# Kernel tuning notes

Measured on AMD Instinct MI355X. Metric: run time of the kernel, lower is better.

## Reference

```python
import jax, jax.numpy as jnp
import numpy as np

N_NODES = 50000


def gcn_conv(x, W, b, row, col, num_nodes):
    """PyG-style GCNConv: out = D^{-1/2}(A+I)D^{-1/2} (x @ W) + b.

    row/col already include self-loops. x: [N, Fin], W: [Fin, Fout].
    """
    h = x @ W  # [N, Fout]
    deg = jax.ops.segment_sum(jnp.ones_like(col, dtype=h.dtype), col,
                              num_segments=num_nodes)  # in-degree incl. self-loop
    dinv = jnp.where(deg > 0, jax.lax.rsqrt(deg), 0.0)
    norm = dinv[row] * dinv[col]  # [E]
    msgs = h[row] * norm[:, None]  # gather + scale, [E, Fout]
    out = jax.ops.segment_sum(msgs, col, num_segments=num_nodes)  # scatter-add
    return out + b


def setup_inputs() -> dict:
    key = jax.random.key(0)
    k1, k2, k3, k4 = jax.random.split(key, 4)
    Fin, Fh, Fout = 128, 128, 64
    E = 800000
    x = jax.random.normal(k1, (N_NODES, Fin), dtype=jnp.float32)
    edge_index = jax.random.randint(k2, (2, E), 0, N_NODES, dtype=jnp.int64)
    # Glorot-ish init for weights
    W1 = jax.random.normal(k3, (Fin, Fh), dtype=jnp.float32) / np.sqrt(Fin)
    b1 = jnp.zeros((Fh,), dtype=jnp.float32)
    W2 = jax.random.normal(k4, (Fh, Fout), dtype=jnp.float32) / np.sqrt(Fh)
    b2 = jnp.zeros((Fout,), dtype=jnp.float32)
    return {"x": x, "edge_index": edge_index, "W1": W1, "b1": b1,
            "W2": W2, "b2": b2}


def reference(x, edge_index, W1, b1, W2, b2):
    n = x.shape[0]
    # add self-loops once (shared by both conv layers)
    loops = jnp.arange(n, dtype=edge_index.dtype)
    row = jnp.concatenate([edge_index[0], loops])
    col = jnp.concatenate([edge_index[1], loops])
    h = jax.nn.relu(gcn_conv(x, W1, b1, row, col, n))
    # dropout(p=0.5) is identity in eval mode (self.training == False)
    return gcn_conv(h, W2, b2, row, col, n)
```

## Files before the change

### kernel.cpp

```cpp
#include <hip/hip_runtime.h>


constexpr int KD = 128;
constexpr int CHUNK = 2048;
constexpr int BCAP = 6144;

using short8  = __attribute__((ext_vector_type(8))) short;
using float4v = __attribute__((ext_vector_type(4))) float;
using uint4v  = __attribute__((ext_vector_type(4))) unsigned int;


__device__ __forceinline__ unsigned short f2bf(float f) {
    unsigned int u = __float_as_uint(f);
    u = (u + 0x7fffu + ((u >> 16) & 1u)) >> 16;
    return (unsigned short)u;
}

__device__ __forceinline__ float2 bfpair(unsigned int u) {
    float2 f;
    f.x = __uint_as_float(u << 16);
    f.y = __uint_as_float(u & 0xffff0000u);
    return f;
}

__device__ __forceinline__ unsigned int packbf(float x, float y) {
    return (unsigned int)f2bf(x) | ((unsigned int)f2bf(y) << 16);
}

__device__ __forceinline__ void bfsplit(float x, unsigned short& h, unsigned short& l) {
    h = f2bf(x);
    float fh = __uint_as_float((unsigned int)h << 16);
    l = f2bf(x - fh);
}

__global__ __launch_bounds__(256) void scatter_setup(
        const int* __restrict__ row, const int* __restrict__ col,
        int* gcur, unsigned int* __restrict__ bpack, int E, int NBS,
        const float* __restrict__ W1, unsigned short* __restrict__ Wth1,
        unsigned short* __restrict__ Wtl1,
        const float* __restrict__ W2, unsigned short* __restrict__ Wth2,
        unsigned short* __restrict__ Wtl2) {
    __shared__ int lh[256];
    __shared__ int lbase[256];

    if ((int)blockIdx.x >= NBS) {
        int id = ((int)blockIdx.x - NBS) * 256 + threadIdx.x;
        unsigned short h, l;
        if (id < 16384) {
            int k = id >> 7, n = id & 127;
            bfsplit(W1[id], h, l);
            Wth1[n * KD + k] = h;
            Wtl1[n * KD + k] = l;
        } else {
            int id2 = id - 16384;
            int k = id2 >> 6, n = id2 & 63;
            bfsplit(W2[id2], h, l);
            Wth2[n * KD + k] = h;
            Wtl2[n * KD + k] = l;
        }
        return;
    }

    lh[threadIdx.x] = 0;
    __syncthreads();
    int base = (int)blockIdx.x * CHUNK;
#pragma unroll
    for (int r = 0; r < CHUNK / 256; ++r) {
        int e = base + r * 256 + threadIdx.x;
        if (e < E) atomicAdd(&lh[col[e] >> 8], 1);
    }
    __syncthreads();
    int c0 = lh[threadIdx.x];
    lbase[threadIdx.x] = c0 ? (threadIdx.x * BCAP + atomicAdd(&gcur[threadIdx.x], c0)) : 0;
    __syncthreads();
    lh[threadIdx.x] = 0;
    __syncthreads();
#pragma unroll
    for (int r = 0; r < CHUNK / 256; ++r) {
        int e = base + r * 256 + threadIdx.x;
        if (e < E) {
            int c = col[e];
            int b = c >> 8;
            int slot = lbase[b] + atomicAdd(&lh[b], 1);
            bpack[slot] = ((unsigned int)row[e] << 16) | (unsigned int)c;
        }
    }
}

__global__ __launch_bounds__(256) void csr_and_gemm1(
        const unsigned int* __restrict__ bpack, const int* __restrict__ gcur,
        int* __restrict__ rowptrS, float* __restrict__ dinv,
        unsigned short* __restrict__ srow, int N, int E, int NBUCKET,
        const float* __restrict__ X,
        const unsigned short* __restrict__ Wth,
        const unsigned short* __restrict__ Wtl,
        unsigned short* __restrict__ G) {
    __shared__ int s[256];
    __shared__ int lh[1024];
    __shared__ int lcur[1024];
    __shared__ int sh_bstart;

    if ((int)blockIdx.x < NBUCKET) {
        int b = blockIdx.x;
        int t = threadIdx.x;
        int cntb = gcur[t];
        s[t] = cntb;
        __syncthreads();
        for (int off = 1; off < 256; off <<= 1) {
            int tv = (t >= off) ? s[t - off] : 0;
            __syncthreads();
            s[t] += tv;
            __syncthreads();
        }
        if (t == b) sh_bstart = s[t] - cntb;
        if (b == 0 && t == 0) rowptrS[4 * N] = E;
#pragma unroll
        for (int k = 0; k < 4; ++k) lh[t * 4 + k] = 0;
        __syncthreads();
        int bstart = sh_bstart;
        int nE = gcur[b];
        int base = b * BCAP;
        for (int i = t; i < nE; i += 256) {
            unsigned int p = bpack[base + i];
            atomicAdd(&lh[(p & 255) * 4 + (p >> 30)], 1);
        }
        __syncthreads();
        int e0 = lh[t * 4], e1 = lh[t * 4 + 1], e2 = lh[t * 4 + 2], e3 = lh[t * 4 + 3];
        int v = e0 + e1 + e2 + e3;
        s[t] = v;
        __syncthreads();
        for (int off = 1; off < 256; off <<= 1) {
            int tv = (t >= off) ? s[t - off] : 0;
            __syncthreads();
            s[t] += tv;
            __syncthreads();
        }
        int myStart = bstart + s[t] - v;
        int node = (b << 8) + t;
        if (node < N) {
            rowptrS[node * 4 + 0] = myStart;
            rowptrS[node * 4 + 1] = myStart + e0;
            rowptrS[node * 4 + 2] = myStart + e0 + e1;
            rowptrS[node * 4 + 3] = myStart + e0 + e1 + e2;
            dinv[node] = rsqrtf(1.0f + (float)v);
        }
        lcur[t * 4 + 0] = myStart;
        lcur[t * 4 + 1] = myStart + e0;
        lcur[t * 4 + 2] = myStart + e0 + e1;
        lcur[t * 4 + 3] = myStart + e0 + e1 + e2;
        __syncthreads();
        for (int i = t; i < nE; i += 256) {
            unsigned int p = bpack[base + i];
            int slot = atomicAdd(&lcur[(p & 255) * 4 + (p >> 30)], 1);
            srow[slot] = (unsigned short)(p >> 16);
        }
    } else {
        constexpr int FOUT = 128, NT = 8;
        int wave = threadIdx.x >> 6;
        int lane = threadIdx.x & 63;
        int row0 = (((int)blockIdx.x - NBUCKET) * 4 + wave) * 16;
        if (row0 >= N) return;
        int m = lane & 15;
        int quad = lane >> 4;

        float4v acc[NT];
#pragma unroll
        for (int ct = 0; ct < NT; ++ct) acc[ct] = (float4v){0.f, 0.f, 0.f, 0.f};

        const float* xrow = X + (size_t)(row0 + m) * KD + quad * 8;

#pragma unroll
        for (int ks = 0; ks < 4; ++ks) {
            float4 xa = *(const float4*)(xrow + ks * 32);
            float4 xb = *(const float4*)(xrow + ks * 32 + 4);
            float xs[8] = {xa.x, xa.y, xa.z, xa.w, xb.x, xb.y, xb.z, xb.w};
            short8 ah, al;
#pragma unroll
            for (int j = 0; j < 8; ++j) {
                unsigned short h, l;
                bfsplit(xs[j], h, l);
                ah[j] = (short)h;
                al[j] = (short)l;
            }
            int koff = ks * 32 + quad * 8;
#pragma unroll
            for (int ct = 0; ct < NT; ++ct) {
                short8 bh = *(const short8*)(Wth + (size_t)(ct * 16 + m) * KD + koff);
                short8 bl = *(const short8*)(Wtl + (size_t)(ct * 16 + m) * KD + koff);
                acc[ct] = __builtin_amdgcn_mfma_f32_16x16x32_bf16(ah, bh, acc[ct], 0, 0, 0);
                acc[ct] = __builtin_amdgcn_mfma_f32_16x16x32_bf16(al, bh, acc[ct], 0, 0, 0);
                acc[ct] = __builtin_amdgcn_mfma_f32_16x16x32_bf16(ah, bl, acc[ct], 0, 0, 0);
            }
        }

#pragma unroll
        for (int r = 0; r < 4; ++r) {
            int row = row0 + quad * 4 + r;
#pragma unroll
            for (int ct = 0; ct < NT; ++ct) {
                G[(size_t)row * FOUT + ct * 16 + m] = f2bf(acc[ct][r]);
            }
        }
    }
}

__global__ __launch_bounds__(256, 4) void gather128_gemm2_seg(
        const int* __restrict__ rowptrS,
        const unsigned short* __restrict__ srow,
        const unsigned int* __restrict__ G,
        const float* __restrict__ dinv,
        const float* __restrict__ bias,
        const unsigned short* __restrict__ Wth,
        const unsigned short* __restrict__ Wtl,
        unsigned short* __restrict__ G2,
        int N, int E) {
    __shared__ unsigned int lhs[16 * 64];
    __shared__ float ldinv[16];

    int lane = threadIdx.x & 63;
    int l16  = threadIdx.x & 15;
    int q    = threadIdx.x >> 4;
    const uint4v* Gv = (const uint4v*)G;

    float acc[4][8];
    float dns[4];

#pragma unroll
    for (int t = 0; t < 4; ++t) {
        int node = (int)blockIdx.x * 64 + t * 16 + q;
        int nc = (node < N) ? node : 0;
        float dn = dinv[nc];
        dns[t] = dn;
        uint4v s0 = Gv[(size_t)nc * 16 + l16];
        float2 v0 = bfpair(s0[0]), v1 = bfpair(s0[1]);
        float2 v2 = bfpair(s0[2]), v3 = bfpair(s0[3]);
        acc[t][0] = v0.x * dn; acc[t][1] = v0.y * dn;
        acc[t][2] = v1.x * dn; acc[t][3] = v1.y * dn;
        acc[t][4] = v2.x * dn; acc[t][5] = v2.y * dn;
        acc[t][6] = v3.x * dn; acc[t][7] = v3.y * dn;
    }

    for (int sgm = 0; sgm < 4; ++sgm) {
#pragma unroll
        for (int t = 0; t < 4; ++t) {
            int node = (int)blockIdx.x * 64 + t * 16 + q;
            bool valid = node < N;
            int nc = valid ? node : 0;
            int beg = rowptrS[nc * 4 + sgm];
            int end = rowptrS[nc * 4 + sgm + 1];
            int deg = valid ? (end - beg) : 0;
            int dm = max(deg, __shfl_xor(deg, 16));
            dm = max(dm, __shfl_xor(dm, 32));
            for (int w = 0; w < dm; w += 16) {
                int li = w + l16;
                li = (li < deg) ? li : (deg > 0 ? deg - 1 : 0);
                li += beg;
                li = (li < E) ? li : (E - 1);
                int rv = (int)srow[li];
                float dv = dinv[rv];
                int lim = dm - w;
                for (int g = 0; g < 16 && g < lim; g += 4) {
                    uint4v u[4];
                    float dr[4];
#pragma unroll
                    for (int j = 0; j < 4; ++j) {
                        int src = (lane & 48) | (g + j);
                        int r = __shfl(rv, src);
                        dr[j] = __shfl(dv, src);
                        u[j] = Gv[(size_t)r * 16 + l16];
                    }
                    float sa[8] = {0.f, 0.f, 0.f, 0.f, 0.f, 0.f, 0.f, 0.f};
#pragma unroll
                    for (int j = 0; j < 4; ++j) {
                        bool ok = (w + g + j) < deg;
#pragma unroll
                        for (int c = 0; c < 4; ++c) {
                            unsigned int uv = ok ? u[j][c] : 0u;
                            float2 v = bfpair(uv);
                            sa[2 * c]     = fmaf(dr[j], v.x, sa[2 * c]);
                            sa[2 * c + 1] = fmaf(dr[j], v.y, sa[2 * c + 1]);
                        }
                    }
#pragma unroll
                    for (int c = 0; c < 8; ++c) acc[t][c] += sa[c];
                }
            }
        }
    }

#pragma unroll
    for (int t = 0; t < 4; ++t) {
        {
            float dn = dns[t];
            if (l16 == 0) ldinv[q] = dn;
            float4 bv0 = ((const float4*)bias)[l16 * 2];
            float4 bv1 = ((const float4*)bias)[l16 * 2 + 1];
            float o[8];
            o[0] = acc[t][0] * dn + bv0.x; o[1] = acc[t][1] * dn + bv0.y;
            o[2] = acc[t][2] * dn + bv0.z; o[3] = acc[t][3] * dn + bv0.w;
            o[4] = acc[t][4] * dn + bv1.x; o[5] = acc[t][5] * dn + bv1.y;
            o[6] = acc[t][6] * dn + bv1.z; o[7] = acc[t][7] * dn + bv1.w;
#pragma unroll
            for (int c = 0; c < 8; ++c) o[c] = fmaxf(o[c], 0.f);
            int lb = q * 64 + l16 * 4;
            lhs[lb + 0] = packbf(o[0], o[1]);
            lhs[lb + 1] = packbf(o[2], o[3]);
            lhs[lb + 2] = packbf(o[4], o[5]);
            lhs[lb + 3] = packbf(o[6], o[7]);
        }
        __syncthreads();
        {
            int ct = threadIdx.x >> 6;
            int m = lane & 15;
            int quad = lane >> 4;
            float4v fa = (float4v){0.f, 0.f, 0.f, 0.f};
#pragma unroll
            for (int ks = 0; ks < 4; ++ks) {
                short8 a = *(const short8*)&lhs[m * 64 + ks * 16 + quad * 4];
                int koff = ks * 32 + quad * 8;
                short8 bh = *(const short8*)(Wth + (size_t)(ct * 16 + m) * KD + koff);
                short8 bl = *(const short8*)(Wtl + (size_t)(ct * 16 + m) * KD + koff);
                fa = __builtin_amdgcn_mfma_f32_16x16x32_bf16(a, bh, fa, 0, 0, 0);
                fa = __builtin_amdgcn_mfma_f32_16x16x32_bf16(a, bl, fa, 0, 0, 0);
            }
#pragma unroll
            for (int r = 0; r < 4; ++r) {
                int rr = quad * 4 + r;
                int gnode = (int)blockIdx.x * 64 + t * 16 + rr;
                if (gnode < N) {
                    G2[(size_t)gnode * 64 + ct * 16 + m] = f2bf(fa[r] * ldinv[rr]);
                }
            }
        }
        __syncthreads();
    }
}

template <bool RELU>
__global__ __launch_bounds__(256) void gather64(const int* __restrict__ rowptrS,
                                                const unsigned short* __restrict__ srow,
                                                const unsigned int* __restrict__ G,
                                                const float* __restrict__ dinv,
                                                const float* __restrict__ bias,
                                                float* __restrict__ O, int N, int E) {
    int tid = blockIdx.x * 256 + (int)threadIdx.x;
    int node = tid >> 4;
    int lane = threadIdx.x & 63;
    int l16 = lane & 15;
    bool valid = node < N;
    int nc = valid ? node : (N - 1);
    int beg = rowptrS[nc * 4];
    int end = rowptrS[nc * 4 + 4];
    int deg = valid ? (end - beg) : 0;

    uint2 s0 = ((const uint2*)G)[(size_t)nc * 16 + l16];
    float2 p0 = bfpair(s0.x), p1 = bfpair(s0.y);
    float ax = p0.x, ay = p0.y, az = p1.x, aw = p1.y;

    int dm = max(deg, __shfl_xor(deg, 16));
    dm = max(dm, __shfl_xor(dm, 32));

    for (int w = 0; w < dm; w += 16) {
        int li = w + l16;
        li = (li < deg) ? li : (deg > 0 ? deg - 1 : 0);
        li += beg;
        li = (li < E) ? li : (E - 1);
        int rv = (int)srow[li];
        int lim = dm - w;
        for (int g = 0; g < 16 && g < lim; g += 8) {
            uint2 u[8];
#pragma unroll
            for (int j = 0; j < 8; ++j) {
                int src = (lane & 48) | (g + j);
                int r = __shfl(rv, src);
                u[j] = ((const uint2*)G)[(size_t)r * 16 + l16];
            }
            float sx = 0.f, sy = 0.f, sz = 0.f, sw = 0.f;
#pragma unroll
            for (int j = 0; j < 8; ++j) {
                bool ok = (w + g + j) < deg;
                unsigned int ux = ok ? u[j].x : 0u;
                unsigned int uy = ok ? u[j].y : 0u;
                float2 v0 = bfpair(ux), v1 = bfpair(uy);
                sx += v0.x; sy += v0.y; sz += v1.x; sw += v1.y;
            }
            ax += sx; ay += sy; az += sz; aw += sw;
        }
    }
    if (!valid) return;
    float s = dinv[nc];
    float4 bv = ((const float4*)bias)[l16];
    float ox = ax * s + bv.x;
    float oy = ay * s + bv.y;
    float oz = az * s + bv.z;
    float ow = aw * s + bv.w;
    if (RELU) {
        ox = fmaxf(ox, 0.f); oy = fmaxf(oy, 0.f);
        oz = fmaxf(oz, 0.f); ow = fmaxf(ow, 0.f);
    }
    float4v o = {ox, oy, oz, ow};
    __builtin_nontemporal_store(o, (float4v*)O + (size_t)nc * 16 + l16);
}

extern "C" void kernel_launch(void* const* d_in, const int* in_sizes, int n_in,
                              void* d_out, int out_size, void* d_ws, size_t ws_size,
                              hipStream_t stream) {
    const float* x  = (const float*)d_in[0];
    const int*   ei = (const int*)d_in[1];
    const float* W1 = (const float*)d_in[2];
    const float* b1 = (const float*)d_in[3];
    const float* W2 = (const float*)d_in[4];
    const float* b2 = (const float*)d_in[5];
    float* out = (float*)d_out;

    int N = in_sizes[0] / 128;
    int E = in_sizes[1] / 2;
    const int* row = ei;
    const int* col = ei + E;

    char* ws = (char*)d_ws;
    float* dinv    = (float*)(ws + 0x000000);
    int*   rowptrS = (int*)  (ws + 0x080000);
    int*   gcur    = (int*)  (ws + 0x150000);
    unsigned short* srow = (unsigned short*)(ws + 0x160000);
    unsigned short* g1 = (unsigned short*)(ws + 0x440000);
    unsigned short* wth1 = (unsigned short*)(ws + 0x10C0000);
    unsigned short* wtl1 = (unsigned short*)(ws + 0x10D0000);
    unsigned short* wth2 = (unsigned short*)(ws + 0x10E0000);
    unsigned short* wtl2 = (unsigned short*)(ws + 0x10F0000);
    unsigned int* bpack = (unsigned int*)(ws + 0x1200000);
    unsigned short* g2 = (unsigned short*)(ws + 0x2C00000);

    int NB_BKT  = (E + CHUNK - 1) / CHUNK;
    int NBUCKET = (N + 255) / 256;
    int NB_GEMM1 = (N + 63) / 64;
    int NB_SETUP = 96;

    hipMemsetAsync(gcur, 0, 256 * sizeof(int), stream);
    scatter_setup<<<NB_BKT + NB_SETUP, 256, 0, stream>>>(
        row, col, gcur, bpack, E, NB_BKT, W1, wth1, wtl1, W2, wth2, wtl2);
    csr_and_gemm1<<<NBUCKET + NB_GEMM1, 256, 0, stream>>>(
        bpack, gcur, rowptrS, dinv, srow, N, E, NBUCKET, x, wth1, wtl1, g1);

    int nb;
    nb = (N + 63) / 64;
    gather128_gemm2_seg<<<nb, 256, 0, stream>>>(rowptrS, srow,
                                                (const unsigned int*)g1,
                                                dinv, b1, wth2, wtl2, g2, N, E);

    nb = (N + 15) / 16;
    gather64<false><<<nb, 256, 0, stream>>>(rowptrS, srow, (const unsigned int*)g2,
                                            dinv, b2, out, N, E);
}
```

Measured before the change: 191.2 us.

## Process 16 nodes per block in layer-1 gather without segment loop

Restructures the layer-1 gather+GEMM2 kernel so each block handles 16 nodes instead of 64, and walks each node's full neighbor range at once instead of looping over four source-sorted segments. It also widens the in-flight gather batch from 4 to 8 rows per lane and drops the occupancy hint from launch_bounds. The intent is more blocks for better load balance, more memory-level parallelism per lane and less loop overhead. The trade-off is losing whatever cache locality the segment ordering gave, and re-reading the weight tiles once per 16 nodes instead of once per 64.

```diff
diff --git a/kernel.cpp b/kernel.cpp
--- a/kernel.cpp
+++ b/kernel.cpp
@@ -204,7 +204,7 @@
     }
 }
 
-__global__ __launch_bounds__(256, 4) void gather128_gemm2_seg(
+__global__ __launch_bounds__(256) void gather128_gemm2(
         const int* __restrict__ rowptrS,
         const unsigned short* __restrict__ srow,
         const unsigned int* __restrict__ G,
@@ -218,121 +218,108 @@
     __shared__ float ldinv[16];
 
     int lane = threadIdx.x & 63;
-    int l16  = threadIdx.x & 15;
-    int q    = threadIdx.x >> 4;
+    int l16 = threadIdx.x & 15;
+    int q = threadIdx.x >> 4;
+    int node = (int)blockIdx.x * 16 + q;
+    bool valid = node < N;
+    int nc = valid ? node : 0;
+    int beg = rowptrS[nc * 4];
+    int end = rowptrS[nc * 4 + 4];
+    int deg = valid ? (end - beg) : 0;
+    float dn = dinv[nc];
+    if (l16 == 0) ldinv[q] = dn;
+
     const uint4v* Gv = (const uint4v*)G;
 
-    float acc[4][8];
-    float dns[4];
-
-#pragma unroll
-    for (int t = 0; t < 4; ++t) {
-        int node = (int)blockIdx.x * 64 + t * 16 + q;
-        int nc = (node < N) ? node : 0;
-        float dn = dinv[nc];
-        dns[t] = dn;
-        uint4v s0 = Gv[(size_t)nc * 16 + l16];
+    uint4v s0 = Gv[(size_t)nc * 16 + l16];
+    float ac[8];
+    {
         float2 v0 = bfpair(s0[0]), v1 = bfpair(s0[1]);
         float2 v2 = bfpair(s0[2]), v3 = bfpair(s0[3]);
-        acc[t][0] = v0.x * dn; acc[t][1] = v0.y * dn;
-        acc[t][2] = v1.x * dn; acc[t][3] = v1.y * dn;
-        acc[t][4] = v2.x * dn; acc[t][5] = v2.y * dn;
-        acc[t][6] = v3.x * dn; acc[t][7] = v3.y * dn;
-    }
-
-    for (int sgm = 0; sgm < 4; ++sgm) {
-#pragma unroll
-        for (int t = 0; t < 4; ++t) {
-            int node = (int)blockIdx.x * 64 + t * 16 + q;
-            bool valid = node < N;
-            int nc = valid ? node : 0;
-            int beg = rowptrS[nc * 4 + sgm];
-            int end = rowptrS[nc * 4 + sgm + 1];
-            int deg = valid ? (end - beg) : 0;
-            int dm = max(deg, __shfl_xor(deg, 16));
-            dm = max(dm, __shfl_xor(dm, 32));
-            for (int w = 0; w < dm; w += 16) {
-                int li = w + l16;
-                li = (li < deg) ? li : (deg > 0 ? deg - 1 : 0);
-                li += beg;
-                li = (li < E) ? li : (E - 1);
-                int rv = (int)srow[li];
-                float dv = dinv[rv];
-                int lim = dm - w;
-                for (int g = 0; g < 16 && g < lim; g += 4) {
-                    uint4v u[4];
-                    float dr[4];
-#pragma unroll
-                    for (int j = 0; j < 4; ++j) {
-                        int src = (lane & 48) | (g + j);
-                        int r = __shfl(rv, src);
-                        dr[j] = __shfl(dv, src);
-                        u[j] = Gv[(size_t)r * 16 + l16];
-                    }
-                    float sa[8] = {0.f, 0.f, 0.f, 0.f, 0.f, 0.f, 0.f, 0.f};
-#pragma unroll
-                    for (int j = 0; j < 4; ++j) {
-                        bool ok = (w + g + j) < deg;
-#pragma unroll
-                        for (int c = 0; c < 4; ++c) {
-                            unsigned int uv = ok ? u[j][c] : 0u;
-                            float2 v = bfpair(uv);
-                            sa[2 * c]     = fmaf(dr[j], v.x, sa[2 * c]);
-                            sa[2 * c + 1] = fmaf(dr[j], v.y, sa[2 * c + 1]);
-                        }
-                    }
-#pragma unroll
-                    for (int c = 0; c < 8; ++c) acc[t][c] += sa[c];
+        ac[0] = v0.x * dn; ac[1] = v0.y * dn;
+        ac[2] = v1.x * dn; ac[3] = v1.y * dn;
+        ac[4] = v2.x * dn; ac[5] = v2.y * dn;
+        ac[6] = v3.x * dn; ac[7] = v3.y * dn;
+    }
+
+    int dm = max(deg, __shfl_xor(deg, 16));
+    dm = max(dm, __shfl_xor(dm, 32));
+
+    for (int w = 0; w < dm; w += 16) {
+        int li = w + l16;
+        li = (li < deg) ? li : (deg > 0 ? deg - 1 : 0);
+        li += beg;
+        li = (li < E) ? li : (E - 1);
+        int rv = (int)srow[li];
+        float dv = dinv[rv];
+        int lim = dm - w;
+        for (int g = 0; g < 16 && g < lim; g += 8) {
+            uint4v u[8];
+            float dr[8];
+#pragma unroll
+            for (int j = 0; j < 8; ++j) {
+                int src = (lane & 48) | (g + j);
+                int r = __shfl(rv, src);
+                dr[j] = __shfl(dv, src);
+                u[j] = Gv[(size_t)r * 16 + l16];
+            }
+            float sa[8] = {0.f, 0.f, 0.f, 0.f, 0.f, 0.f, 0.f, 0.f};
+#pragma unroll
+            for (int j = 0; j < 8; ++j) {
+                bool ok = (w + g + j) < deg;
+#pragma unroll
+                for (int c = 0; c < 4; ++c) {
+                    unsigned int uv = ok ? u[j][c] : 0u;
+                    float2 v = bfpair(uv);
+                    sa[2 * c]     = fmaf(dr[j], v.x, sa[2 * c]);
+                    sa[2 * c + 1] = fmaf(dr[j], v.y, sa[2 * c + 1]);
                 }
             }
-        }
-    }
-
-#pragma unroll
-    for (int t = 0; t < 4; ++t) {
-        {
-            float dn = dns[t];
-            if (l16 == 0) ldinv[q] = dn;
-            float4 bv0 = ((const float4*)bias)[l16 * 2];
-            float4 bv1 = ((const float4*)bias)[l16 * 2 + 1];
-            float o[8];
-            o[0] = acc[t][0] * dn + bv0.x; o[1] = acc[t][1] * dn + bv0.y;
-            o[2] = acc[t][2] * dn + bv0.z; o[3] = acc[t][3] * dn + bv0.w;
-            o[4] = acc[t][4] * dn + bv1.x; o[5] = acc[t][5] * dn + bv1.y;
-            o[6] = acc[t][6] * dn + bv1.z; o[7] = acc[t][7] * dn + bv1.w;
-#pragma unroll
-            for (int c = 0; c < 8; ++c) o[c] = fmaxf(o[c], 0.f);
-            int lb = q * 64 + l16 * 4;
-            lhs[lb + 0] = packbf(o[0], o[1]);
-            lhs[lb + 1] = packbf(o[2], o[3]);
-            lhs[lb + 2] = packbf(o[4], o[5]);
-            lhs[lb + 3] = packbf(o[6], o[7]);
-        }
-        __syncthreads();
-        {
-            int ct = threadIdx.x >> 6;
-            int m = lane & 15;
-            int quad = lane >> 4;
-            float4v fa = (float4v){0.f, 0.f, 0.f, 0.f};
-#pragma unroll
-            for (int ks = 0; ks < 4; ++ks) {
-                short8 a = *(const short8*)&lhs[m * 64 + ks * 16 + quad * 4];
-                int koff = ks * 32 + quad * 8;
-                short8 bh = *(const short8*)(Wth + (size_t)(ct * 16 + m) * KD + koff);
-                short8 bl = *(const short8*)(Wtl + (size_t)(ct * 16 + m) * KD + koff);
-                fa = __builtin_amdgcn_mfma_f32_16x16x32_bf16(a, bh, fa, 0, 0, 0);
-                fa = __builtin_amdgcn_mfma_f32_16x16x32_bf16(a, bl, fa, 0, 0, 0);
-            }
-#pragma unroll
-            for (int r = 0; r < 4; ++r) {
-                int rr = quad * 4 + r;
-                int gnode = (int)blockIdx.x * 64 + t * 16 + rr;
-                if (gnode < N) {
-                    G2[(size_t)gnode * 64 + ct * 16 + m] = f2bf(fa[r] * ldinv[rr]);
-                }
-            }
-        }
-        __syncthreads();
+#pragma unroll
+            for (int c = 0; c < 8; ++c) ac[c] += sa[c];
+        }
+    }
+
+    {
+        float4 bv0 = ((const float4*)bias)[l16 * 2];
+        float4 bv1 = ((const float4*)bias)[l16 * 2 + 1];
+        float o[8];
+        o[0] = ac[0] * dn + bv0.x; o[1] = ac[1] * dn + bv0.y;
+        o[2] = ac[2] * dn + bv0.z; o[3] = ac[3] * dn + bv0.w;
+        o[4] = ac[4] * dn + bv1.x; o[5] = ac[5] * dn + bv1.y;
+        o[6] = ac[6] * dn + bv1.z; o[7] = ac[7] * dn + bv1.w;
+#pragma unroll
+        for (int c = 0; c < 8; ++c) o[c] = fmaxf(o[c], 0.f);
+        int lb = q * 64 + l16 * 4;
+        lhs[lb + 0] = packbf(o[0], o[1]);
+        lhs[lb + 1] = packbf(o[2], o[3]);
+        lhs[lb + 2] = packbf(o[4], o[5]);
+        lhs[lb + 3] = packbf(o[6], o[7]);
+    }
+    __syncthreads();
+
+    int ct = threadIdx.x >> 6;
+    int m = lane & 15;
+    int quad = lane >> 4;
+
+    float4v acc = (float4v){0.f, 0.f, 0.f, 0.f};
+#pragma unroll
+    for (int ks = 0; ks < 4; ++ks) {
+        short8 a = *(const short8*)&lhs[m * 64 + ks * 16 + quad * 4];
+        int koff = ks * 32 + quad * 8;
+        short8 bh = *(const short8*)(Wth + (size_t)(ct * 16 + m) * KD + koff);
+        short8 bl = *(const short8*)(Wtl + (size_t)(ct * 16 + m) * KD + koff);
+        acc = __builtin_amdgcn_mfma_f32_16x16x32_bf16(a, bh, acc, 0, 0, 0);
+        acc = __builtin_amdgcn_mfma_f32_16x16x32_bf16(a, bl, acc, 0, 0, 0);
+    }
+
+#pragma unroll
+    for (int r = 0; r < 4; ++r) {
+        int rr = quad * 4 + r;
+        int gnode = (int)blockIdx.x * 16 + rr;
+        if (gnode < N) {
+            G2[(size_t)gnode * 64 + ct * 16 + m] = f2bf(acc[r] * ldinv[rr]);
+        }
     }
 }
 
@@ -443,10 +430,9 @@
         bpack, gcur, rowptrS, dinv, srow, N, E, NBUCKET, x, wth1, wtl1, g1);
 
     int nb;
-    nb = (N + 63) / 64;
-    gather128_gemm2_seg<<<nb, 256, 0, stream>>>(rowptrS, srow,
-                                                (const unsigned int*)g1,
-                                                dinv, b1, wth2, wtl2, g2, N, E);
+    nb = (N + 15) / 16;
+    gather128_gemm2<<<nb, 256, 0, stream>>>(rowptrS, srow, (const unsigned int*)g1,
+                                            dinv, b1, wth2, wtl2, g2, N, E);
 
     nb = (N + 15) / 16;
     gather64<false><<<nb, 256, 0, stream>>>(rowptrS, srow, (const unsigned int*)g2,
```

Result: faster. 183.4 us (-4.1%).
